# Kernel optimization log

Measured on AMD Instinct MI355X. Metric: run time of the kernel, lower is better.

## Reference

```python
import jax, jax.numpy as jnp
import numpy as np

B, QL, ML = 8, 128, 1024
QS, KS, H = 512, 512, 256


def setup_inputs() -> dict:
    key = jax.random.key(0)
    ks = jax.random.split(key, 10)
    query = jax.random.normal(ks[0], (B, QL, QS), dtype=jnp.float32)
    memory = jax.random.normal(ks[1], (B, ML, KS), dtype=jnp.float32)
    mask = jax.random.bernoulli(ks[2], 0.1, (B, ML))
    mask = mask.at[:, 0].set(False)  # ensure at least one valid position per row
    s_q = 1.0 / np.sqrt(QS)
    s_k = 1.0 / np.sqrt(KS)
    s_h = 1.0 / np.sqrt(H)
    Wq = jax.random.uniform(ks[3], (H, QS), jnp.float32, -s_q, s_q)
    bq = jax.random.uniform(ks[4], (H,), jnp.float32, -s_q, s_q)
    Wk = jax.random.uniform(ks[5], (H, KS), jnp.float32, -s_k, s_k)
    bk = jax.random.uniform(ks[6], (H,), jnp.float32, -s_k, s_k)
    wl = jax.random.uniform(ks[7], (H,), jnp.float32, -s_h, s_h)
    bl = jax.random.uniform(ks[8], (), jnp.float32, -s_h, s_h)
    return {"query": query, "memory": memory, "mask": mask,
            "Wq": Wq, "bq": bq, "Wk": Wk, "bk": bk, "wl": wl, "bl": bl}


def reference(query, memory, mask, Wq, bq, Wk, bk, wl, bl):
    # q: [B, QL, H], k: [B, ML, H]
    q = jnp.einsum('bqs,hs->bqh', query, Wq) + bq
    k = jnp.einsum('bms,hs->bmh', memory, Wk) + bk
    # additive score: tanh(q + k) projected to scalar  -> [B, QL, ML]
    z = jnp.tanh(q[:, :, None, :] + k[:, None, :, :])  # [B, QL, ML, H]
    logits = jnp.einsum('bqmh,h->bqm', z, wl) + bl
    logits = jnp.where(mask[:, None, :], jnp.float32(-1e18), logits)
    weights = jax.nn.softmax(logits, axis=-1)  # BottleSoftmax over mem_len
    attns = jnp.einsum('bqm,bms->bqs', weights, memory)
    return attns, weights
```

## Files before the change

### kernel.cpp

```cpp
#include <hip/hip_runtime.h>

#define B_  8
#define QL_ 128
#define ML_ 1024
#define KS_ 512
#define H_  256

#define QP_OFF 0
#define KP_OFF 262144
#define MASK_OFF 2359296
#define WH_OFF 2361344
#define WL_OFF 2492416

typedef __attribute__((ext_vector_type(8))) short bfrag;
typedef __attribute__((ext_vector_type(4))) float f4acc;

__device__ __forceinline__ void split1(float v, unsigned& h, unsigned& lo) {
    unsigned u  = __float_as_uint(v);
    unsigned hb = u & 0xFFFF0000u;
    float    lf = v - __uint_as_float(hb);
    unsigned ul = __float_as_uint(lf);
    unsigned lr = ul + 0x7FFFu + ((ul >> 16) & 1u);
    h  = u >> 16;
    lo = lr >> 16;
}

__device__ __forceinline__ void split4(const float4& a, unsigned& h01, unsigned& h23,
                                       unsigned& l01, unsigned& l23) {
    unsigned h[4], l[4];
    split1(a.x, h[0], l[0]); split1(a.y, h[1], l[1]);
    split1(a.z, h[2], l[2]); split1(a.w, h[3], l[3]);
    h01 = h[0] | (h[1] << 16); h23 = h[2] | (h[3] << 16);
    l01 = l[0] | (l[1] << 16); l23 = l[2] | (l[3] << 16);
}

__global__ __launch_bounds__(256) void prep_kernel(
    const float* __restrict__ Wq, const float* __restrict__ Wk,
    unsigned short* __restrict__ Whi, unsigned short* __restrict__ Wlo,
    const unsigned char* __restrict__ mraw, unsigned char* __restrict__ mout) {
    const int bid = blockIdx.x;
    const int t = threadIdx.x;

    if (bid == 64) {
        __shared__ int s_not01, s_not0f;
        const unsigned int* w = (const unsigned int*)mraw;
        if (t == 0) { s_not01 = 0; s_not0f = 0; }
        __syncthreads();
        int not01 = 0, not0f = 0;
        for (int i = t; i < 2048; i += 256) {
            unsigned int v = w[i];
            if (v != 0u && v != 1u) not01 = 1;
            if (v != 0u && v != 0x3F800000u) not0f = 1;
        }
        if (not01) atomicOr(&s_not01, 1);
        if (not0f) atomicOr(&s_not0f, 1);
        __syncthreads();
        int wordTyped = (!s_not01) || (!s_not0f);
        for (int i = t; i < B_ * ML_; i += 256) {
            unsigned char mv;
            if (wordTyped) mv = (w[i] != 0u) ? 1 : 0;
            else           mv = mraw[i] ? 1 : 0;
            mout[i] = mv;
        }
        return;
    }

    const float* src = (bid < 32) ? Wq : Wk;
    const int lb = bid & 31;
    const size_t loff = (size_t)lb * 4096 + (size_t)t * 16;
    const size_t doff = ((bid < 32) ? 0 : 131072) + loff;

    unsigned hw[8], lw[8];
#pragma unroll
    for (int i = 0; i < 4; ++i) {
        float4 v = *(const float4*)(src + loff + i * 4);
        split4(v, hw[i * 2], hw[i * 2 + 1], lw[i * 2], lw[i * 2 + 1]);
    }
    *(uint4*)(Whi + doff)     = make_uint4(hw[0], hw[1], hw[2], hw[3]);
    *(uint4*)(Whi + doff + 8) = make_uint4(hw[4], hw[5], hw[6], hw[7]);
    *(uint4*)(Wlo + doff)     = make_uint4(lw[0], lw[1], lw[2], lw[3]);
    *(uint4*)(Wlo + doff + 8) = make_uint4(lw[4], lw[5], lw[6], lw[7]);
}

__global__ __launch_bounds__(256) void proj_kernel(
    const float* __restrict__ query, const float* __restrict__ memory,
    const unsigned short* __restrict__ Whi, const unsigned short* __restrict__ Wlo,
    const float* __restrict__ bq, const float* __restrict__ bk,
    float* __restrict__ Eq, float* __restrict__ Ek) {
    const int bid = blockIdx.x;
    const int t = threadIdx.x;
    const int nb = bid & 1;
    const int mb = bid >> 1;

    const float *X, *bias; float* out; int row0, wbase0;
    if (mb < 32) { X = query;  bias = bq; out = Eq; row0 = mb * 32;        wbase0 = 0; }
    else         { X = memory; bias = bk; out = Ek; row0 = (mb - 32) * 32; wbase0 = 256; }

    const int w  = t >> 6;
    const int l  = t & 63;
    const int lr = l & 15;
    const int lk = l >> 4;

    const int arow = t >> 3;
    const int acol = (t & 7) << 2;
    const float* Xp = X + (size_t)(row0 + arow) * 512 + acol;
    __shared__ unsigned int AH[2][32][16];
    __shared__ unsigned int AL[2][32][16];
    const int wg  = ((t & 7) >> 1) ^ ((arow >> 1) & 3);
    const int wwo = ((t & 7) & 1) << 1;

    const int wrow0 = wbase0 + nb * 128 + w * 32;
    const unsigned short* bhP0 = Whi + (size_t)(wrow0 + 0 * 16 + lr) * 512 + lk * 8;
    const unsigned short* bhP1 = Whi + (size_t)(wrow0 + 1 * 16 + lr) * 512 + lk * 8;
    const unsigned short* blP0 = Wlo + (size_t)(wrow0 + 0 * 16 + lr) * 512 + lk * 8;
    const unsigned short* blP1 = Wlo + (size_t)(wrow0 + 1 * 16 + lr) * 512 + lk * 8;

    f4acc acc[2][2];
#pragma unroll
    for (int mi = 0; mi < 2; ++mi)
#pragma unroll
        for (int ni = 0; ni < 2; ++ni)
            acc[mi][ni] = (f4acc){0.f, 0.f, 0.f, 0.f};

#define WRA(P, XA) do {                                               \
    unsigned h01, h23, l01, l23;                                      \
    split4(XA, h01, h23, l01, l23);                                   \
    unsigned int* dh = &AH[P][arow][wg * 4 + wwo];                    \
    unsigned int* dl = &AL[P][arow][wg * 4 + wwo];                    \
    dh[0] = h01; dh[1] = h23; dl[0] = l01; dl[1] = l23; } while (0)

#define LDB(BH0, BH1, BL0, BL1, c) do {                               \
    BH0 = *(const uint4*)(bhP0 + (size_t)(c) * 32);                   \
    BH1 = *(const uint4*)(bhP1 + (size_t)(c) * 32);                   \
    BL0 = *(const uint4*)(blP0 + (size_t)(c) * 32);                   \
    BL1 = *(const uint4*)(blP1 + (size_t)(c) * 32); } while (0)

#define COMP(P, BH0, BH1, BL0, BL1) do {                              \
    bfrag ah[2], al[2];                                               \
    _Pragma("unroll")                                                 \
    for (int mi = 0; mi < 2; ++mi) {                                  \
        int ra = mi * 16 + lr;                                        \
        int g4 = (lk ^ ((ra >> 1) & 3)) * 4;                          \
        ah[mi] = *(const bfrag*)&AH[P][ra][g4];                       \
        al[mi] = *(const bfrag*)&AL[P][ra][g4];                       \
    }                                                                 \
    bfrag bh[2], bl[2];                                               \
    bh[0] = __builtin_bit_cast(bfrag, BH0);                           \
    bh[1] = __builtin_bit_cast(bfrag, BH1);                           \
    bl[0] = __builtin_bit_cast(bfrag, BL0);                           \
    bl[1] = __builtin_bit_cast(bfrag, BL1);                           \
    _Pragma("unroll")                                                 \
    for (int mi = 0; mi < 2; ++mi)                                    \
    _Pragma("unroll")                                                 \
    for (int ni = 0; ni < 2; ++ni) {                                  \
        acc[mi][ni] = __builtin_amdgcn_mfma_f32_16x16x32_bf16(        \
            ah[mi], bh[ni], acc[mi][ni], 0, 0, 0);                    \
        acc[mi][ni] = __builtin_amdgcn_mfma_f32_16x16x32_bf16(        \
            ah[mi], bl[ni], acc[mi][ni], 0, 0, 0);                    \
        acc[mi][ni] = __builtin_amdgcn_mfma_f32_16x16x32_bf16(        \
            al[mi], bh[ni], acc[mi][ni], 0, 0, 0);                    \
    } } while (0)

    float4 xa0 = *(const float4*)(Xp);
    uint4 bh00, bh01, bl00, bl01;
    LDB(bh00, bh01, bl00, bl01, 0);
    float4 xa1 = *(const float4*)(Xp + 32);
    uint4 bh10, bh11, bl10, bl11;
    LDB(bh10, bh11, bl10, bl11, 1);
    WRA(0, xa0);
    __syncthreads();

    for (int c2 = 0; c2 < 8; ++c2) {
        WRA(1, xa1);
        if (c2 < 7) xa0 = *(const float4*)(Xp + (2 * c2 + 2) * 32);
        COMP(0, bh00, bh01, bl00, bl01);
        if (c2 < 7) LDB(bh00, bh01, bl00, bl01, 2 * c2 + 2);
        __syncthreads();
        if (c2 < 7) WRA(0, xa0);
        COMP(1, bh10, bh11, bl10, bl11);
        if (c2 < 7) {
            xa1 = *(const float4*)(Xp + (2 * c2 + 3) * 32);
            LDB(bh10, bh11, bl10, bl11, 2 * c2 + 3);
        }
        __syncthreads();
    }
#undef WRA
#undef LDB
#undef COMP

    const float SC = 2.885390081777926815f;
    float bcol[2];
#pragma unroll
    for (int ni = 0; ni < 2; ++ni) bcol[ni] = bias[nb * 128 + w * 32 + ni * 16 + lr];

#pragma unroll
    for (int mi = 0; mi < 2; ++mi)
#pragma unroll
        for (int ni = 0; ni < 2; ++ni) {
            const int col = nb * 128 + w * 32 + ni * 16 + lr;
#pragma unroll
            for (int r = 0; r < 4; ++r) {
                const int row = row0 + mi * 16 + lk * 4 + r;
                out[(size_t)row * 256 + col] =
                    __builtin_amdgcn_exp2f(SC * (acc[mi][ni][r] + bcol[ni]));
            }
        }
}

__global__ __launch_bounds__(256) void logits_kernel(
    const float* __restrict__ Eq, const float* __restrict__ Ek,
    const float* __restrict__ wl, float* __restrict__ sr) {
    const int bid = blockIdx.x;
    const int b  = bid & 7;
    const int r2 = bid >> 3;
    const int mt = r2 & 7;
    const int qt = r2 >> 3;
    const int tid = threadIdx.x;
    const int m  = tid & 127;
    const int qh = tid >> 7;

    __shared__ float eqs[2048];
    __shared__ float wls[256];
    __shared__ float kq[4][128][4];

    const float* qpb = Eq + ((size_t)(b * QL_ + qt * 8)) * H_;
    const float* kpb = Ek + ((size_t)(b * ML_ + mt * 128)) * H_;

    *(float4*)(&eqs[tid * 4])        = *(const float4*)(qpb + tid * 4);
    *(float4*)(&eqs[1024 + tid * 4]) = *(const float4*)(qpb + 1024 + tid * 4);
    if (tid < 64) *(float4*)(&wls[tid * 4]) = *(const float4*)(wl + tid * 4);

    const int srow = tid & 127;
    const int sq2  = tid >> 7;
    const float* kst = kpb + (size_t)srow * H_ + 8 * sq2;
    float4 a0 = *(const float4*)(kst);
    float4 a1 = *(const float4*)(kst + 4);

    float acc[4] = {0.f, 0.f, 0.f, 0.f};

    for (int c = 0; c < 16; ++c) {
        __syncthreads();
        *(float4*)(&kq[2 * sq2 + 0][srow][0]) = a0;
        *(float4*)(&kq[2 * sq2 + 1][srow][0]) = a1;
        __syncthreads();
        if (c < 15) {
            a0 = *(const float4*)(kst + (c + 1) * 16);
            a1 = *(const float4*)(kst + (c + 1) * 16 + 4);
        }
        const int h0 = c * 16;
#pragma unroll
        for (int quad = 0; quad < 4; ++quad) {
            float4 k4 = *(const float4*)(&kq[quad][m][0]);
            float4 w4 = *(const float4*)(&wls[h0 + quad * 4]);
#pragma unroll
            for (int j2 = 0; j2 < 4; ++j2) {
                float4 q4 = *(const float4*)(&eqs[(qh * 4 + j2) * 256 + h0 + quad * 4]);
                float p0 = fmaf(k4.x, q4.x, 1.0f);
                float p1 = fmaf(k4.y, q4.y, 1.0f);
                float p2 = fmaf(k4.z, q4.z, 1.0f);
                float p3 = fmaf(k4.w, q4.w, 1.0f);
                float p01 = p0 * p1, p23 = p2 * p3;
                float n01 = fmaf(w4.y, p0, w4.x * p1);
                float n23 = fmaf(w4.w, p2, w4.z * p3);
                float Nm  = fmaf(n23, p01, n01 * p23);
                float P   = p01 * p23;
                acc[j2] = fmaf(Nm, __builtin_amdgcn_rcpf(P), acc[j2]);
            }
        }
    }
#pragma unroll
    for (int j2 = 0; j2 < 4; ++j2)
        sr[((size_t)(b * QL_ + qt * 8 + qh * 4 + j2)) * ML_ + mt * 128 + m] = acc[j2];
}

__global__ __launch_bounds__(256) void softmax_kernel(
    float* __restrict__ wrow_io, const unsigned char* __restrict__ mv) {
    const int row = blockIdx.x;
    const int b = row >> 7;
    const int tid = threadIdx.x;
    float* srow = wrow_io + (size_t)row * ML_;
    const unsigned char* mrow = mv + b * ML_;
    __shared__ float red[4];

    float4 s4 = *(const float4*)(srow + tid * 4);
    uchar4 m4 = *(const uchar4*)(mrow + tid * 4);
    float l[4];
    l[0] = m4.x ? -1e18f : -2.0f * s4.x;
    l[1] = m4.y ? -1e18f : -2.0f * s4.y;
    l[2] = m4.z ? -1e18f : -2.0f * s4.z;
    l[3] = m4.w ? -1e18f : -2.0f * s4.w;

    float mx = fmaxf(fmaxf(l[0], l[1]), fmaxf(l[2], l[3]));
#pragma unroll
    for (int off = 32; off >= 1; off >>= 1)
        mx = fmaxf(mx, __shfl_xor(mx, off));
    if ((tid & 63) == 0) red[tid >> 6] = mx;
    __syncthreads();
    mx = fmaxf(fmaxf(red[0], red[1]), fmaxf(red[2], red[3]));
    __syncthreads();

    const float L2E = 1.44269504088896340736f;
    float e[4], s = 0.f;
#pragma unroll
    for (int i = 0; i < 4; ++i) {
        e[i] = __builtin_amdgcn_exp2f((l[i] - mx) * L2E);
        s += e[i];
    }
#pragma unroll
    for (int off = 32; off >= 1; off >>= 1)
        s += __shfl_xor(s, off);
    if ((tid & 63) == 0) red[tid >> 6] = s;
    __syncthreads();
    s = (red[0] + red[1]) + (red[2] + red[3]);
    float inv = __builtin_amdgcn_rcpf(s);
    float4 o = make_float4(e[0] * inv, e[1] * inv, e[2] * inv, e[3] * inv);
    *(float4*)(srow + tid * 4) = o;
}

__global__ __launch_bounds__(256) void attn_out_kernel(
    const float* __restrict__ wgt, const float* __restrict__ mem,
    float* __restrict__ out) {
    const int bid = blockIdx.x;
    const int b  = bid & 7;
    const int j2 = bid >> 3;
    const int mt = j2 & 3;
    const int nt = j2 >> 2;
    const int t = threadIdx.x;
    __shared__ float As[32][34];
    __shared__ float Bs[32][64];

    const int ar = t >> 3, ac = (t & 7) << 2;
    const int br = t >> 4, bc = (t & 15) << 2;
    const float* Ap = wgt + ((size_t)(b * QL_ + mt * 32 + ar)) * ML_ + ac;
    const float* Bp = mem + ((size_t)(b * ML_ + br)) * KS_ + nt * 64 + bc;

    const int tx = t & 15, ty = t >> 4;
    float acc0[4] = {0.f, 0.f, 0.f, 0.f};
    float acc1[4] = {0.f, 0.f, 0.f, 0.f};

    float4 apre = *(const float4*)(Ap);
    float4 bpre0 = *(const float4*)(Bp);
    float4 bpre1 = *(const float4*)(Bp + (size_t)16 * KS_);

    for (int k0 = 0; k0 < ML_; k0 += 32) {
        __syncthreads();
        As[ac + 0][ar] = apre.x; As[ac + 1][ar] = apre.y;
        As[ac + 2][ar] = apre.z; As[ac + 3][ar] = apre.w;
        *(float4*)(&Bs[br][bc])      = bpre0;
        *(float4*)(&Bs[br + 16][bc]) = bpre1;
        __syncthreads();
        if (k0 + 32 < ML_) {
            apre  = *(const float4*)(Ap + k0 + 32);
            bpre0 = *(const float4*)(Bp + (size_t)(k0 + 32) * KS_);
            bpre1 = *(const float4*)(Bp + (size_t)(k0 + 48) * KS_);
        }
#pragma unroll
        for (int kk = 0; kk < 32; ++kk) {
            float2 a2 = *(const float2*)(&As[kk][ty * 2]);
            float4 b4 = *(const float4*)(&Bs[kk][tx * 4]);
            acc0[0] = fmaf(a2.x, b4.x, acc0[0]);
            acc0[1] = fmaf(a2.x, b4.y, acc0[1]);
            acc0[2] = fmaf(a2.x, b4.z, acc0[2]);
            acc0[3] = fmaf(a2.x, b4.w, acc0[3]);
            acc1[0] = fmaf(a2.y, b4.x, acc1[0]);
            acc1[1] = fmaf(a2.y, b4.y, acc1[1]);
            acc1[2] = fmaf(a2.y, b4.z, acc1[2]);
            acc1[3] = fmaf(a2.y, b4.w, acc1[3]);
        }
    }
    size_t orow = ((size_t)(b * QL_ + mt * 32 + ty * 2)) * KS_ + nt * 64 + tx * 4;
    *(float4*)(out + orow)       = make_float4(acc0[0], acc0[1], acc0[2], acc0[3]);
    *(float4*)(out + orow + KS_) = make_float4(acc1[0], acc1[1], acc1[2], acc1[3]);
}

extern "C" void kernel_launch(void* const* d_in, const int* in_sizes, int n_in,
                              void* d_out, int out_size, void* d_ws, size_t ws_size,
                              hipStream_t stream) {
    const float* query  = (const float*)d_in[0];
    const float* memory = (const float*)d_in[1];
    const unsigned char* mask = (const unsigned char*)d_in[2];
    const float* Wq = (const float*)d_in[3];
    const float* bq = (const float*)d_in[4];
    const float* Wk = (const float*)d_in[5];
    const float* bk = (const float*)d_in[6];
    const float* wl = (const float*)d_in[7];

    float* ws = (float*)d_ws;
    float* Eq = ws + QP_OFF;
    float* Ek = ws + KP_OFF;
    unsigned char* mcan = (unsigned char*)(ws + MASK_OFF);
    unsigned short* Whi = (unsigned short*)(ws + WH_OFF);
    unsigned short* Wlo = (unsigned short*)(ws + WL_OFF);

    float* attns = (float*)d_out;
    float* wout  = (float*)d_out + B_ * QL_ * KS_;

    prep_kernel<<<dim3(65),  dim3(256), 0, stream>>>(Wq, Wk, Whi, Wlo, mask, mcan);
    proj_kernel<<<dim3(576), dim3(256), 0, stream>>>(query, memory, Whi, Wlo,
                                                     bq, bk, Eq, Ek);
    logits_kernel<<<dim3(1024), dim3(256), 0, stream>>>(Eq, Ek, wl, wout);
    softmax_kernel<<<dim3(B_ * QL_), dim3(256), 0, stream>>>(wout, mcan);
    attn_out_kernel<<<dim3(256), dim3(256), 0, stream>>>(wout, memory, attns);
}
```

Measured before the change: 187.1 us.

## Pre-split activations to bf16 hi/lo, drop LDS in projection, double-buffer logits

The prep kernel now also splits query and memory into bf16 hi/lo arrays in workspace, so the projection kernel loads both MFMA operands straight from global memory with no LDS staging or barriers. The projection uses 64x64 tiles with a block-index swizzle across XCDs. The logits kernel double-buffers the K tile in LDS, leaving one barrier per step, and reads q and wl directly from global memory instead of staging them in shared memory. This trades extra global traffic (writing and re-reading the split activations) for fewer syncs and less split work inside the GEMM.

After: 201.6 us. +7.7%, slower.

```diff
diff --git a/kernel.cpp b/kernel.cpp
--- a/kernel.cpp
+++ b/kernel.cpp
@@ -11,6 +11,8 @@
 #define MASK_OFF 2359296
 #define WH_OFF 2361344
 #define WL_OFF 2492416
+#define XH_OFF 2623488
+#define XL_OFF 4982784
 
 typedef __attribute__((ext_vector_type(8))) short bfrag;
 typedef __attribute__((ext_vector_type(4))) float f4acc;
@@ -35,13 +37,15 @@
 }
 
 __global__ __launch_bounds__(256) void prep_kernel(
+    const float* __restrict__ query, const float* __restrict__ memory,
     const float* __restrict__ Wq, const float* __restrict__ Wk,
     unsigned short* __restrict__ Whi, unsigned short* __restrict__ Wlo,
+    unsigned short* __restrict__ Xhi, unsigned short* __restrict__ Xlo,
     const unsigned char* __restrict__ mraw, unsigned char* __restrict__ mout) {
     const int bid = blockIdx.x;
     const int t = threadIdx.x;
 
-    if (bid == 64) {
+    if (bid == 1216) {
         __shared__ int s_not01, s_not0f;
         const unsigned int* w = (const unsigned int*)mraw;
         if (t == 0) { s_not01 = 0; s_not0f = 0; }
@@ -65,55 +69,65 @@
         return;
     }
 
-    const float* src = (bid < 32) ? Wq : Wk;
-    const int lb = bid & 31;
-    const size_t loff = (size_t)lb * 4096 + (size_t)t * 16;
-    const size_t doff = ((bid < 32) ? 0 : 131072) + loff;
+    const float* src; unsigned short *dh, *dl; size_t soff, doff;
+    if (bid < 64) {
+        src = (bid < 32) ? Wq : Wk;
+        soff = (size_t)(bid & 31) * 4096;
+        doff = ((bid < 32) ? 0 : 131072) + soff;
+        dh = Whi; dl = Wlo;
+    } else if (bid < 192) {
+        src = query;  soff = (size_t)(bid - 64) * 4096;  doff = soff;
+        dh = Xhi; dl = Xlo;
+    } else {
+        src = memory; soff = (size_t)(bid - 192) * 4096; doff = 524288 + soff;
+        dh = Xhi; dl = Xlo;
+    }
+    soff += (size_t)t * 16; doff += (size_t)t * 16;
 
     unsigned hw[8], lw[8];
 #pragma unroll
     for (int i = 0; i < 4; ++i) {
-        float4 v = *(const float4*)(src + loff + i * 4);
+        float4 v = *(const float4*)(src + soff + i * 4);
         split4(v, hw[i * 2], hw[i * 2 + 1], lw[i * 2], lw[i * 2 + 1]);
     }
-    *(uint4*)(Whi + doff)     = make_uint4(hw[0], hw[1], hw[2], hw[3]);
-    *(uint4*)(Whi + doff + 8) = make_uint4(hw[4], hw[5], hw[6], hw[7]);
-    *(uint4*)(Wlo + doff)     = make_uint4(lw[0], lw[1], lw[2], lw[3]);
-    *(uint4*)(Wlo + doff + 8) = make_uint4(lw[4], lw[5], lw[6], lw[7]);
+    *(uint4*)(dh + doff)     = make_uint4(hw[0], hw[1], hw[2], hw[3]);
+    *(uint4*)(dh + doff + 8) = make_uint4(hw[4], hw[5], hw[6], hw[7]);
+    *(uint4*)(dl + doff)     = make_uint4(lw[0], lw[1], lw[2], lw[3]);
+    *(uint4*)(dl + doff + 8) = make_uint4(lw[4], lw[5], lw[6], lw[7]);
 }
 
 __global__ __launch_bounds__(256) void proj_kernel(
-    const float* __restrict__ query, const float* __restrict__ memory,
+    const unsigned short* __restrict__ Xhi, const unsigned short* __restrict__ Xlo,
     const unsigned short* __restrict__ Whi, const unsigned short* __restrict__ Wlo,
     const float* __restrict__ bq, const float* __restrict__ bk,
     float* __restrict__ Eq, float* __restrict__ Ek) {
     const int bid = blockIdx.x;
     const int t = threadIdx.x;
-    const int nb = bid & 1;
-    const int mb = bid >> 1;
-
-    const float *X, *bias; float* out; int row0, wbase0;
-    if (mb < 32) { X = query;  bias = bq; out = Eq; row0 = mb * 32;        wbase0 = 0; }
-    else         { X = memory; bias = bk; out = Ek; row0 = (mb - 32) * 32; wbase0 = 256; }
+    const int wk = (bid & 7) * 72 + (bid >> 3);
+    const int nb = wk & 3;
+    const int mb = wk >> 2;
+
+    const bool isQ = (mb < 16);
+    const int arow0 = mb * 64;
+    const int orow0 = isQ ? mb * 64 : mb * 64 - 1024;
+    const float* bias = isQ ? bq : bk;
+    float* out = isQ ? Eq : Ek;
+    const int wrb = (isQ ? 0 : 256) + nb * 64;
 
     const int w  = t >> 6;
+    const int wm = w >> 1, wn = w & 1;
     const int l  = t & 63;
     const int lr = l & 15;
     const int lk = l >> 4;
 
-    const int arow = t >> 3;
-    const int acol = (t & 7) << 2;
-    const float* Xp = X + (size_t)(row0 + arow) * 512 + acol;
-    __shared__ unsigned int AH[2][32][16];
-    __shared__ unsigned int AL[2][32][16];
-    const int wg  = ((t & 7) >> 1) ^ ((arow >> 1) & 3);
-    const int wwo = ((t & 7) & 1) << 1;
-
-    const int wrow0 = wbase0 + nb * 128 + w * 32;
-    const unsigned short* bhP0 = Whi + (size_t)(wrow0 + 0 * 16 + lr) * 512 + lk * 8;
-    const unsigned short* bhP1 = Whi + (size_t)(wrow0 + 1 * 16 + lr) * 512 + lk * 8;
-    const unsigned short* blP0 = Wlo + (size_t)(wrow0 + 0 * 16 + lr) * 512 + lk * 8;
-    const unsigned short* blP1 = Wlo + (size_t)(wrow0 + 1 * 16 + lr) * 512 + lk * 8;
+    const unsigned short* pah0 = Xhi + (size_t)(arow0 + wm * 32 +  0 + lr) * 512 + lk * 8;
+    const unsigned short* pah1 = Xhi + (size_t)(arow0 + wm * 32 + 16 + lr) * 512 + lk * 8;
+    const unsigned short* pal0 = Xlo + (size_t)(arow0 + wm * 32 +  0 + lr) * 512 + lk * 8;
+    const unsigned short* pal1 = Xlo + (size_t)(arow0 + wm * 32 + 16 + lr) * 512 + lk * 8;
+    const unsigned short* pbh0 = Whi + (size_t)(wrb + wn * 32 +  0 + lr) * 512 + lk * 8;
+    const unsigned short* pbh1 = Whi + (size_t)(wrb + wn * 32 + 16 + lr) * 512 + lk * 8;
+    const unsigned short* pbl0 = Wlo + (size_t)(wrb + wn * 32 +  0 + lr) * 512 + lk * 8;
+    const unsigned short* pbl1 = Wlo + (size_t)(wrb + wn * 32 + 16 + lr) * 512 + lk * 8;
 
     f4acc acc[2][2];
 #pragma unroll
@@ -122,33 +136,29 @@
         for (int ni = 0; ni < 2; ++ni)
             acc[mi][ni] = (f4acc){0.f, 0.f, 0.f, 0.f};
 
-#define WRA(P, XA) do {                                               \
-    unsigned h01, h23, l01, l23;                                      \
-    split4(XA, h01, h23, l01, l23);                                   \
-    unsigned int* dh = &AH[P][arow][wg * 4 + wwo];                    \
-    unsigned int* dl = &AL[P][arow][wg * 4 + wwo];                    \
-    dh[0] = h01; dh[1] = h23; dl[0] = l01; dl[1] = l23; } while (0)
-
-#define LDB(BH0, BH1, BL0, BL1, c) do {                               \
-    BH0 = *(const uint4*)(bhP0 + (size_t)(c) * 32);                   \
-    BH1 = *(const uint4*)(bhP1 + (size_t)(c) * 32);                   \
-    BL0 = *(const uint4*)(blP0 + (size_t)(c) * 32);                   \
-    BL1 = *(const uint4*)(blP1 + (size_t)(c) * 32); } while (0)
-
-#define COMP(P, BH0, BH1, BL0, BL1) do {                              \
-    bfrag ah[2], al[2];                                               \
-    _Pragma("unroll")                                                 \
-    for (int mi = 0; mi < 2; ++mi) {                                  \
-        int ra = mi * 16 + lr;                                        \
-        int g4 = (lk ^ ((ra >> 1) & 3)) * 4;                          \
-        ah[mi] = *(const bfrag*)&AH[P][ra][g4];                       \
-        al[mi] = *(const bfrag*)&AL[P][ra][g4];                       \
-    }                                                                 \
-    bfrag bh[2], bl[2];                                               \
-    bh[0] = __builtin_bit_cast(bfrag, BH0);                           \
-    bh[1] = __builtin_bit_cast(bfrag, BH1);                           \
-    bl[0] = __builtin_bit_cast(bfrag, BL0);                           \
-    bl[1] = __builtin_bit_cast(bfrag, BL1);                           \
+    uint4 s0ah0, s0ah1, s0al0, s0al1, s0bh0, s0bh1, s0bl0, s0bl1;
+    uint4 s1ah0, s1ah1, s1al0, s1al1, s1bh0, s1bh1, s1bl0, s1bl1;
+
+#define LDSET(P, c) do {                                              \
+    P##ah0 = *(const uint4*)(pah0 + (size_t)(c) * 32);                \
+    P##ah1 = *(const uint4*)(pah1 + (size_t)(c) * 32);                \
+    P##al0 = *(const uint4*)(pal0 + (size_t)(c) * 32);                \
+    P##al1 = *(const uint4*)(pal1 + (size_t)(c) * 32);                \
+    P##bh0 = *(const uint4*)(pbh0 + (size_t)(c) * 32);                \
+    P##bh1 = *(const uint4*)(pbh1 + (size_t)(c) * 32);                \
+    P##bl0 = *(const uint4*)(pbl0 + (size_t)(c) * 32);                \
+    P##bl1 = *(const uint4*)(pbl1 + (size_t)(c) * 32); } while (0)
+
+#define COMPSET(P) do {                                               \
+    bfrag ah[2], al[2], bh[2], bl[2];                                 \
+    ah[0] = __builtin_bit_cast(bfrag, P##ah0);                        \
+    ah[1] = __builtin_bit_cast(bfrag, P##ah1);                        \
+    al[0] = __builtin_bit_cast(bfrag, P##al0);                        \
+    al[1] = __builtin_bit_cast(bfrag, P##al1);                        \
+    bh[0] = __builtin_bit_cast(bfrag, P##bh0);                        \
+    bh[1] = __builtin_bit_cast(bfrag, P##bh1);                        \
+    bl[0] = __builtin_bit_cast(bfrag, P##bl0);                        \
+    bl[1] = __builtin_bit_cast(bfrag, P##bl1);                        \
     _Pragma("unroll")                                                 \
     for (int mi = 0; mi < 2; ++mi)                                    \
     _Pragma("unroll")                                                 \
@@ -161,46 +171,31 @@
             al[mi], bh[ni], acc[mi][ni], 0, 0, 0);                    \
     } } while (0)
 
-    float4 xa0 = *(const float4*)(Xp);
-    uint4 bh00, bh01, bl00, bl01;
-    LDB(bh00, bh01, bl00, bl01, 0);
-    float4 xa1 = *(const float4*)(Xp + 32);
-    uint4 bh10, bh11, bl10, bl11;
-    LDB(bh10, bh11, bl10, bl11, 1);
-    WRA(0, xa0);
-    __syncthreads();
-
+    LDSET(s0, 0);
+    LDSET(s1, 1);
+#pragma unroll
     for (int c2 = 0; c2 < 8; ++c2) {
-        WRA(1, xa1);
-        if (c2 < 7) xa0 = *(const float4*)(Xp + (2 * c2 + 2) * 32);
-        COMP(0, bh00, bh01, bl00, bl01);
-        if (c2 < 7) LDB(bh00, bh01, bl00, bl01, 2 * c2 + 2);
-        __syncthreads();
-        if (c2 < 7) WRA(0, xa0);
-        COMP(1, bh10, bh11, bl10, bl11);
-        if (c2 < 7) {
-            xa1 = *(const float4*)(Xp + (2 * c2 + 3) * 32);
-            LDB(bh10, bh11, bl10, bl11, 2 * c2 + 3);
-        }
-        __syncthreads();
-    }
-#undef WRA
-#undef LDB
-#undef COMP
+        COMPSET(s0);
+        if (c2 < 7) LDSET(s0, 2 * c2 + 2);
+        COMPSET(s1);
+        if (c2 < 7) LDSET(s1, 2 * c2 + 3);
+    }
+#undef LDSET
+#undef COMPSET
 
     const float SC = 2.885390081777926815f;
     float bcol[2];
 #pragma unroll
-    for (int ni = 0; ni < 2; ++ni) bcol[ni] = bias[nb * 128 + w * 32 + ni * 16 + lr];
+    for (int ni = 0; ni < 2; ++ni) bcol[ni] = bias[nb * 64 + wn * 32 + ni * 16 + lr];
 
 #pragma unroll
     for (int mi = 0; mi < 2; ++mi)
 #pragma unroll
         for (int ni = 0; ni < 2; ++ni) {
-            const int col = nb * 128 + w * 32 + ni * 16 + lr;
+            const int col = nb * 64 + wn * 32 + ni * 16 + lr;
 #pragma unroll
             for (int r = 0; r < 4; ++r) {
-                const int row = row0 + mi * 16 + lk * 4 + r;
+                const int row = orow0 + wm * 32 + mi * 16 + lk * 4 + r;
                 out[(size_t)row * 256 + col] =
                     __builtin_amdgcn_exp2f(SC * (acc[mi][ni][r] + bcol[ni]));
             }
@@ -217,44 +212,45 @@
     const int qt = r2 >> 3;
     const int tid = threadIdx.x;
     const int m  = tid & 127;
-    const int qh = tid >> 7;
-
-    __shared__ float eqs[2048];
-    __shared__ float wls[256];
-    __shared__ float kq[4][128][4];
-
-    const float* qpb = Eq + ((size_t)(b * QL_ + qt * 8)) * H_;
+    const int qh = __builtin_amdgcn_readfirstlane(tid >> 7);
+
+    __shared__ float kq[2][4][128][4];
+
+    const float* qpb = Eq + ((size_t)(b * QL_ + qt * 8 + qh * 4)) * H_;
     const float* kpb = Ek + ((size_t)(b * ML_ + mt * 128)) * H_;
-
-    *(float4*)(&eqs[tid * 4])        = *(const float4*)(qpb + tid * 4);
-    *(float4*)(&eqs[1024 + tid * 4]) = *(const float4*)(qpb + 1024 + tid * 4);
-    if (tid < 64) *(float4*)(&wls[tid * 4]) = *(const float4*)(wl + tid * 4);
 
     const int srow = tid & 127;
     const int sq2  = tid >> 7;
     const float* kst = kpb + (size_t)srow * H_ + 8 * sq2;
+
     float4 a0 = *(const float4*)(kst);
     float4 a1 = *(const float4*)(kst + 4);
+    *(float4*)(&kq[0][2 * sq2 + 0][srow][0]) = a0;
+    *(float4*)(&kq[0][2 * sq2 + 1][srow][0]) = a1;
+    a0 = *(const float4*)(kst + 16);
+    a1 = *(const float4*)(kst + 20);
+    __syncthreads();
 
     float acc[4] = {0.f, 0.f, 0.f, 0.f};
 
     for (int c = 0; c < 16; ++c) {
-        __syncthreads();
-        *(float4*)(&kq[2 * sq2 + 0][srow][0]) = a0;
-        *(float4*)(&kq[2 * sq2 + 1][srow][0]) = a1;
-        __syncthreads();
+        const int cb = c & 1;
         if (c < 15) {
-            a0 = *(const float4*)(kst + (c + 1) * 16);
-            a1 = *(const float4*)(kst + (c + 1) * 16 + 4);
+            *(float4*)(&kq[cb ^ 1][2 * sq2 + 0][srow][0]) = a0;
+            *(float4*)(&kq[cb ^ 1][2 * sq2 + 1][srow][0]) = a1;
+            if (c < 14) {
+                a0 = *(const float4*)(kst + (c + 2) * 16);
+                a1 = *(const float4*)(kst + (c + 2) * 16 + 4);
+            }
         }
         const int h0 = c * 16;
 #pragma unroll
         for (int quad = 0; quad < 4; ++quad) {
-            float4 k4 = *(const float4*)(&kq[quad][m][0]);
-            float4 w4 = *(const float4*)(&wls[h0 + quad * 4]);
+            float4 k4 = *(const float4*)(&kq[cb][quad][m][0]);
+            float4 w4 = *(const float4*)(wl + h0 + quad * 4);
 #pragma unroll
             for (int j2 = 0; j2 < 4; ++j2) {
-                float4 q4 = *(const float4*)(&eqs[(qh * 4 + j2) * 256 + h0 + quad * 4]);
+                float4 q4 = *(const float4*)(qpb + (size_t)j2 * H_ + h0 + quad * 4);
                 float p0 = fmaf(k4.x, q4.x, 1.0f);
                 float p1 = fmaf(k4.y, q4.y, 1.0f);
                 float p2 = fmaf(k4.z, q4.z, 1.0f);
@@ -267,6 +263,7 @@
                 acc[j2] = fmaf(Nm, __builtin_amdgcn_rcpf(P), acc[j2]);
             }
         }
+        __syncthreads();
     }
 #pragma unroll
     for (int j2 = 0; j2 < 4; ++j2)
@@ -391,12 +388,15 @@
     unsigned char* mcan = (unsigned char*)(ws + MASK_OFF);
     unsigned short* Whi = (unsigned short*)(ws + WH_OFF);
     unsigned short* Wlo = (unsigned short*)(ws + WL_OFF);
+    unsigned short* Xhi = (unsigned short*)(ws + XH_OFF);
+    unsigned short* Xlo = (unsigned short*)(ws + XL_OFF);
 
     float* attns = (float*)d_out;
     float* wout  = (float*)d_out + B_ * QL_ * KS_;
 
-    prep_kernel<<<dim3(65),  dim3(256), 0, stream>>>(Wq, Wk, Whi, Wlo, mask, mcan);
-    proj_kernel<<<dim3(576), dim3(256), 0, stream>>>(query, memory, Whi, Wlo,
+    prep_kernel<<<dim3(1217), dim3(256), 0, stream>>>(query, memory, Wq, Wk,
+                                                      Whi, Wlo, Xhi, Xlo, mask, mcan);
+    proj_kernel<<<dim3(576), dim3(256), 0, stream>>>(Xhi, Xlo, Whi, Wlo,
                                                      bq, bk, Eq, Ek);
     logits_kernel<<<dim3(1024), dim3(256), 0, stream>>>(Eq, Ek, wl, wout);
     softmax_kernel<<<dim3(B_ * QL_), dim3(256), 0, stream>>>(wout, mcan);
```

## Move attention-output GEMM to split-bf16 MFMA and double-buffer logits tiles

Applied to the files above, without the earlier changes.

The weights-times-memory GEMM now runs on bf16 MFMA using a hi/lo split (three products) instead of scalar fp32 FMAs. To feed it, the prep kernel transposes memory and splits it into bf16 hi/lo planes, and softmax writes bf16 hi/lo copies of the weights. The logits kernel double-buffers the K tile in shared memory and reads Eq and wl directly from global memory instead of staging them. The extra transpose and split passes add memory traffic and workspace, and dropping the hi*lo-of-lo terms slightly lowers precision.

Measured after the change: 166.0 us. 1.13x faster.

```diff
diff --git a/kernel.cpp b/kernel.cpp
--- a/kernel.cpp
+++ b/kernel.cpp
@@ -11,6 +11,10 @@
 #define MASK_OFF 2359296
 #define WH_OFF 2361344
 #define WL_OFF 2492416
+#define MT_H_OFF 2623488
+#define MT_L_OFF 4720640
+#define WB_H_OFF 6817792
+#define WB_L_OFF 7342080
 
 typedef __attribute__((ext_vector_type(8))) short bfrag;
 typedef __attribute__((ext_vector_type(4))) float f4acc;
@@ -35,13 +39,15 @@
 }
 
 __global__ __launch_bounds__(256) void prep_kernel(
+    const float* __restrict__ memory,
     const float* __restrict__ Wq, const float* __restrict__ Wk,
     unsigned short* __restrict__ Whi, unsigned short* __restrict__ Wlo,
+    unsigned short* __restrict__ MThi, unsigned short* __restrict__ MTlo,
     const unsigned char* __restrict__ mraw, unsigned char* __restrict__ mout) {
     const int bid = blockIdx.x;
     const int t = threadIdx.x;
 
-    if (bid == 64) {
+    if (bid == 1088) {
         __shared__ int s_not01, s_not0f;
         const unsigned int* w = (const unsigned int*)mraw;
         if (t == 0) { s_not01 = 0; s_not0f = 0; }
@@ -65,21 +71,52 @@
         return;
     }
 
-    const float* src = (bid < 32) ? Wq : Wk;
-    const int lb = bid & 31;
-    const size_t loff = (size_t)lb * 4096 + (size_t)t * 16;
-    const size_t doff = ((bid < 32) ? 0 : 131072) + loff;
-
-    unsigned hw[8], lw[8];
-#pragma unroll
-    for (int i = 0; i < 4; ++i) {
-        float4 v = *(const float4*)(src + loff + i * 4);
-        split4(v, hw[i * 2], hw[i * 2 + 1], lw[i * 2], lw[i * 2 + 1]);
-    }
-    *(uint4*)(Whi + doff)     = make_uint4(hw[0], hw[1], hw[2], hw[3]);
-    *(uint4*)(Whi + doff + 8) = make_uint4(hw[4], hw[5], hw[6], hw[7]);
-    *(uint4*)(Wlo + doff)     = make_uint4(lw[0], lw[1], lw[2], lw[3]);
-    *(uint4*)(Wlo + doff + 8) = make_uint4(lw[4], lw[5], lw[6], lw[7]);
+    if (bid < 64) {
+        const float* src = (bid < 32) ? Wq : Wk;
+        size_t loff = (size_t)(bid & 31) * 4096 + (size_t)t * 16;
+        size_t doff = ((bid < 32) ? 0 : 131072) + loff;
+        unsigned hw[8], lw[8];
+#pragma unroll
+        for (int i = 0; i < 4; ++i) {
+            float4 v = *(const float4*)(src + loff + i * 4);
+            split4(v, hw[i * 2], hw[i * 2 + 1], lw[i * 2], lw[i * 2 + 1]);
+        }
+        *(uint4*)(Whi + doff)     = make_uint4(hw[0], hw[1], hw[2], hw[3]);
+        *(uint4*)(Whi + doff + 8) = make_uint4(hw[4], hw[5], hw[6], hw[7]);
+        *(uint4*)(Wlo + doff)     = make_uint4(lw[0], lw[1], lw[2], lw[3]);
+        *(uint4*)(Wlo + doff + 8) = make_uint4(lw[4], lw[5], lw[6], lw[7]);
+        return;
+    }
+
+    const int idx = bid - 64;
+    const int b  = idx >> 7;
+    const int r  = idx & 127;
+    const int mt = r >> 3;
+    const int st = r & 7;
+    __shared__ float T[64][68];
+
+    const int i  = t >> 2, jb = (t & 3) << 4;
+    const float* mp = memory + ((size_t)(b * ML_ + mt * 64 + i)) * KS_ + st * 64 + jb;
+#pragma unroll
+    for (int q = 0; q < 4; ++q)
+        *(float4*)(&T[i][jb + q * 4]) = *(const float4*)(mp + q * 4);
+    __syncthreads();
+
+    const int s = t >> 2, mb = (t & 3) << 4;
+    unsigned hh[16], ll[16];
+#pragma unroll
+    for (int e = 0; e < 16; ++e) split1(T[mb + e][s], hh[e], ll[e]);
+    unsigned hp[8], lp[8];
+#pragma unroll
+    for (int e = 0; e < 8; ++e) {
+        hp[e] = hh[2 * e] | (hh[2 * e + 1] << 16);
+        lp[e] = ll[2 * e] | (ll[2 * e + 1] << 16);
+    }
+    const size_t doff = ((size_t)(b * KS_ + st * 64 + s)) * ML_ + mt * 64 + mb;
+    *(uint4*)(MThi + doff)     = make_uint4(hp[0], hp[1], hp[2], hp[3]);
+    *(uint4*)(MThi + doff + 8) = make_uint4(hp[4], hp[5], hp[6], hp[7]);
+    *(uint4*)(MTlo + doff)     = make_uint4(lp[0], lp[1], lp[2], lp[3]);
+    *(uint4*)(MTlo + doff + 8) = make_uint4(lp[4], lp[5], lp[6], lp[7]);
 }
 
 __global__ __launch_bounds__(256) void proj_kernel(
@@ -217,44 +254,45 @@
     const int qt = r2 >> 3;
     const int tid = threadIdx.x;
     const int m  = tid & 127;
-    const int qh = tid >> 7;
-
-    __shared__ float eqs[2048];
-    __shared__ float wls[256];
-    __shared__ float kq[4][128][4];
-
-    const float* qpb = Eq + ((size_t)(b * QL_ + qt * 8)) * H_;
+    const int qh = __builtin_amdgcn_readfirstlane(tid >> 7);
+
+    __shared__ float kq[2][4][128][4];
+
+    const float* qpb = Eq + ((size_t)(b * QL_ + qt * 8 + qh * 4)) * H_;
     const float* kpb = Ek + ((size_t)(b * ML_ + mt * 128)) * H_;
-
-    *(float4*)(&eqs[tid * 4])        = *(const float4*)(qpb + tid * 4);
-    *(float4*)(&eqs[1024 + tid * 4]) = *(const float4*)(qpb + 1024 + tid * 4);
-    if (tid < 64) *(float4*)(&wls[tid * 4]) = *(const float4*)(wl + tid * 4);
 
     const int srow = tid & 127;
     const int sq2  = tid >> 7;
     const float* kst = kpb + (size_t)srow * H_ + 8 * sq2;
+
     float4 a0 = *(const float4*)(kst);
     float4 a1 = *(const float4*)(kst + 4);
+    *(float4*)(&kq[0][2 * sq2 + 0][srow][0]) = a0;
+    *(float4*)(&kq[0][2 * sq2 + 1][srow][0]) = a1;
+    a0 = *(const float4*)(kst + 16);
+    a1 = *(const float4*)(kst + 20);
+    __syncthreads();
 
     float acc[4] = {0.f, 0.f, 0.f, 0.f};
 
     for (int c = 0; c < 16; ++c) {
-        __syncthreads();
-        *(float4*)(&kq[2 * sq2 + 0][srow][0]) = a0;
-        *(float4*)(&kq[2 * sq2 + 1][srow][0]) = a1;
-        __syncthreads();
+        const int cb = c & 1;
         if (c < 15) {
-            a0 = *(const float4*)(kst + (c + 1) * 16);
-            a1 = *(const float4*)(kst + (c + 1) * 16 + 4);
+            *(float4*)(&kq[cb ^ 1][2 * sq2 + 0][srow][0]) = a0;
+            *(float4*)(&kq[cb ^ 1][2 * sq2 + 1][srow][0]) = a1;
+            if (c < 14) {
+                a0 = *(const float4*)(kst + (c + 2) * 16);
+                a1 = *(const float4*)(kst + (c + 2) * 16 + 4);
+            }
         }
         const int h0 = c * 16;
 #pragma unroll
         for (int quad = 0; quad < 4; ++quad) {
-            float4 k4 = *(const float4*)(&kq[quad][m][0]);
-            float4 w4 = *(const float4*)(&wls[h0 + quad * 4]);
+            float4 k4 = *(const float4*)(&kq[cb][quad][m][0]);
+            float4 w4 = *(const float4*)(wl + h0 + quad * 4);
 #pragma unroll
             for (int j2 = 0; j2 < 4; ++j2) {
-                float4 q4 = *(const float4*)(&eqs[(qh * 4 + j2) * 256 + h0 + quad * 4]);
+                float4 q4 = *(const float4*)(qpb + (size_t)j2 * H_ + h0 + quad * 4);
                 float p0 = fmaf(k4.x, q4.x, 1.0f);
                 float p1 = fmaf(k4.y, q4.y, 1.0f);
                 float p2 = fmaf(k4.z, q4.z, 1.0f);
@@ -267,6 +305,7 @@
                 acc[j2] = fmaf(Nm, __builtin_amdgcn_rcpf(P), acc[j2]);
             }
         }
+        __syncthreads();
     }
 #pragma unroll
     for (int j2 = 0; j2 < 4; ++j2)
@@ -274,7 +313,8 @@
 }
 
 __global__ __launch_bounds__(256) void softmax_kernel(
-    float* __restrict__ wrow_io, const unsigned char* __restrict__ mv) {
+    float* __restrict__ wrow_io, const unsigned char* __restrict__ mv,
+    unsigned short* __restrict__ Wbhi, unsigned short* __restrict__ Wblo) {
     const int row = blockIdx.x;
     const int b = row >> 7;
     const int tid = threadIdx.x;
@@ -315,62 +355,104 @@
     float inv = __builtin_amdgcn_rcpf(s);
     float4 o = make_float4(e[0] * inv, e[1] * inv, e[2] * inv, e[3] * inv);
     *(float4*)(srow + tid * 4) = o;
+
+    unsigned h01, h23, l01, l23;
+    split4(o, h01, h23, l01, l23);
+    *(uint2*)(Wbhi + (size_t)row * ML_ + tid * 4) = make_uint2(h01, h23);
+    *(uint2*)(Wblo + (size_t)row * ML_ + tid * 4) = make_uint2(l01, l23);
 }
 
 __global__ __launch_bounds__(256) void attn_out_kernel(
-    const float* __restrict__ wgt, const float* __restrict__ mem,
+    const unsigned short* __restrict__ Wbhi, const unsigned short* __restrict__ Wblo,
+    const unsigned short* __restrict__ MThi, const unsigned short* __restrict__ MTlo,
     float* __restrict__ out) {
     const int bid = blockIdx.x;
     const int b  = bid & 7;
-    const int j2 = bid >> 3;
-    const int mt = j2 & 3;
-    const int nt = j2 >> 2;
+    const int r  = bid >> 3;
+    const int mt = r & 7;
+    const int nt = r >> 3;
     const int t = threadIdx.x;
-    __shared__ float As[32][34];
-    __shared__ float Bs[32][64];
-
-    const int ar = t >> 3, ac = (t & 7) << 2;
-    const int br = t >> 4, bc = (t & 15) << 2;
-    const float* Ap = wgt + ((size_t)(b * QL_ + mt * 32 + ar)) * ML_ + ac;
-    const float* Bp = mem + ((size_t)(b * ML_ + br)) * KS_ + nt * 64 + bc;
-
-    const int tx = t & 15, ty = t >> 4;
-    float acc0[4] = {0.f, 0.f, 0.f, 0.f};
-    float acc1[4] = {0.f, 0.f, 0.f, 0.f};
-
-    float4 apre = *(const float4*)(Ap);
-    float4 bpre0 = *(const float4*)(Bp);
-    float4 bpre1 = *(const float4*)(Bp + (size_t)16 * KS_);
-
-    for (int k0 = 0; k0 < ML_; k0 += 32) {
-        __syncthreads();
-        As[ac + 0][ar] = apre.x; As[ac + 1][ar] = apre.y;
-        As[ac + 2][ar] = apre.z; As[ac + 3][ar] = apre.w;
-        *(float4*)(&Bs[br][bc])      = bpre0;
-        *(float4*)(&Bs[br + 16][bc]) = bpre1;
-        __syncthreads();
-        if (k0 + 32 < ML_) {
-            apre  = *(const float4*)(Ap + k0 + 32);
-            bpre0 = *(const float4*)(Bp + (size_t)(k0 + 32) * KS_);
-            bpre1 = *(const float4*)(Bp + (size_t)(k0 + 48) * KS_);
-        }
-#pragma unroll
-        for (int kk = 0; kk < 32; ++kk) {
-            float2 a2 = *(const float2*)(&As[kk][ty * 2]);
-            float4 b4 = *(const float4*)(&Bs[kk][tx * 4]);
-            acc0[0] = fmaf(a2.x, b4.x, acc0[0]);
-            acc0[1] = fmaf(a2.x, b4.y, acc0[1]);
-            acc0[2] = fmaf(a2.x, b4.z, acc0[2]);
-            acc0[3] = fmaf(a2.x, b4.w, acc0[3]);
-            acc1[0] = fmaf(a2.y, b4.x, acc1[0]);
-            acc1[1] = fmaf(a2.y, b4.y, acc1[1]);
-            acc1[2] = fmaf(a2.y, b4.z, acc1[2]);
-            acc1[3] = fmaf(a2.y, b4.w, acc1[3]);
-        }
-    }
-    size_t orow = ((size_t)(b * QL_ + mt * 32 + ty * 2)) * KS_ + nt * 64 + tx * 4;
-    *(float4*)(out + orow)       = make_float4(acc0[0], acc0[1], acc0[2], acc0[3]);
-    *(float4*)(out + orow + KS_) = make_float4(acc1[0], acc1[1], acc1[2], acc1[3]);
+    const int w  = t >> 6;
+    const int l  = t & 63;
+    const int lr = l & 15, lk = l >> 4;
+
+    __shared__ unsigned short As[2][16][2][64];
+    __shared__ unsigned short Bs[2][64][2][64];
+
+    const int pa  = t >> 7;
+    const int ar  = (t >> 3) & 15;
+    const int acq = t & 7;
+    const unsigned short* asrc = (pa ? Wblo : Wbhi)
+        + ((size_t)(b * QL_ + mt * 16 + ar)) * ML_ + acq * 8;
+    const int aws = (acq ^ (ar & 7)) * 8;
+
+    const int pb  = t >> 7;
+    const int br  = (t & 127) >> 1;
+    const int bq0 = (t & 1) * 4;
+    const unsigned short* bsrc = (pb ? MTlo : MThi)
+        + ((size_t)(b * KS_ + nt * 64 + br)) * ML_ + bq0 * 8;
+    int bws[4];
+#pragma unroll
+    for (int i2 = 0; i2 < 4; ++i2) bws[i2] = ((bq0 + i2) ^ (br & 7)) * 8;
+
+    f4acc acc = (f4acc){0.f, 0.f, 0.f, 0.f};
+
+    uint4 g0a, g0b0, g0b1, g0b2, g0b3;
+    uint4 g1a, g1b0, g1b1, g1b2, g1b3;
+
+#define LOADG(G, c) do {                                                  \
+    G##a  = *(const uint4*)(asrc + (size_t)(c) * 64);                     \
+    G##b0 = *(const uint4*)(bsrc + (size_t)(c) * 64);                     \
+    G##b1 = *(const uint4*)(bsrc + (size_t)(c) * 64 + 8);                 \
+    G##b2 = *(const uint4*)(bsrc + (size_t)(c) * 64 + 16);                \
+    G##b3 = *(const uint4*)(bsrc + (size_t)(c) * 64 + 24); } while (0)
+
+#define WRITEB(P, G) do {                                                 \
+    *(uint4*)(&As[P][ar][pa][aws])    = G##a;                             \
+    *(uint4*)(&Bs[P][br][pb][bws[0]]) = G##b0;                            \
+    *(uint4*)(&Bs[P][br][pb][bws[1]]) = G##b1;                            \
+    *(uint4*)(&Bs[P][br][pb][bws[2]]) = G##b2;                            \
+    *(uint4*)(&Bs[P][br][pb][bws[3]]) = G##b3; } while (0)
+
+#define COMPUTE(P) do {                                                   \
+    _Pragma("unroll")                                                     \
+    for (int ks = 0; ks < 2; ++ks) {                                      \
+        const int k8 = (ks * 4 + lk) ^ (lr & 7);                          \
+        bfrag ah = *(const bfrag*)&As[P][lr][0][k8 * 8];                  \
+        bfrag al = *(const bfrag*)&As[P][lr][1][k8 * 8];                  \
+        bfrag bh = *(const bfrag*)&Bs[P][w * 16 + lr][0][k8 * 8];         \
+        bfrag bl = *(const bfrag*)&Bs[P][w * 16 + lr][1][k8 * 8];         \
+        acc = __builtin_amdgcn_mfma_f32_16x16x32_bf16(ah, bh, acc, 0,0,0);\
+        acc = __builtin_amdgcn_mfma_f32_16x16x32_bf16(ah, bl, acc, 0,0,0);\
+        acc = __builtin_amdgcn_mfma_f32_16x16x32_bf16(al, bh, acc, 0,0,0);\
+    } } while (0)
+
+    LOADG(g0, 0);
+    WRITEB(0, g0);
+    LOADG(g1, 1);
+    __syncthreads();
+
+#pragma unroll
+    for (int c = 0; c < 16; ++c) {
+        if (c + 1 < 16) {
+            if ((c + 1) & 1) WRITEB(1, g1); else WRITEB(0, g0);
+        }
+        if (c + 2 < 16) {
+            if (c & 1) LOADG(g1, c + 2); else LOADG(g0, c + 2);
+        }
+        COMPUTE(c & 1);
+        __syncthreads();
+    }
+#undef LOADG
+#undef WRITEB
+#undef COMPUTE
+
+    const int col = nt * 64 + w * 16 + lr;
+#pragma unroll
+    for (int rr = 0; rr < 4; ++rr) {
+        const int row = mt * 16 + lk * 4 + rr;
+        out[((size_t)(b * QL_ + row)) * KS_ + col] = acc[rr];
+    }
 }
 
 extern "C" void kernel_launch(void* const* d_in, const int* in_sizes, int n_in,
@@ -389,16 +471,21 @@
     float* Eq = ws + QP_OFF;
     float* Ek = ws + KP_OFF;
     unsigned char* mcan = (unsigned char*)(ws + MASK_OFF);
-    unsigned short* Whi = (unsigned short*)(ws + WH_OFF);
-    unsigned short* Wlo = (unsigned short*)(ws + WL_OFF);
+    unsigned short* Whi  = (unsigned short*)(ws + WH_OFF);
+    unsigned short* Wlo  = (unsigned short*)(ws + WL_OFF);
+    unsigned short* MThi = (unsigned short*)(ws + MT_H_OFF);
+    unsigned short* MTlo = (unsigned short*)(ws + MT_L_OFF);
+    unsigned short* Wbhi = (unsigned short*)(ws + WB_H_OFF);
+    unsigned short* Wblo = (unsigned short*)(ws + WB_L_OFF);
 
     float* attns = (float*)d_out;
     float* wout  = (float*)d_out + B_ * QL_ * KS_;
 
-    prep_kernel<<<dim3(65),  dim3(256), 0, stream>>>(Wq, Wk, Whi, Wlo, mask, mcan);
+    prep_kernel<<<dim3(1089), dim3(256), 0, stream>>>(memory, Wq, Wk, Whi, Wlo,
+                                                      MThi, MTlo, mask, mcan);
     proj_kernel<<<dim3(576), dim3(256), 0, stream>>>(query, memory, Whi, Wlo,
                                                      bq, bk, Eq, Ek);
     logits_kernel<<<dim3(1024), dim3(256), 0, stream>>>(Eq, Ek, wl, wout);
-    softmax_kernel<<<dim3(B_ * QL_), dim3(256), 0, stream>>>(wout, mcan);
-    attn_out_kernel<<<dim3(256), dim3(256), 0, stream>>>(wout, memory, attns);
-}
+    softmax_kernel<<<dim3(B_ * QL_), dim3(256), 0, stream>>>(wout, mcan, Wbhi, Wblo);
+    attn_out_kernel<<<dim3(512), dim3(256), 0, stream>>>(Wbhi, Wblo, MThi, MTlo, attns);
+}
```
